# Kernel optimization log

Hardware: AMD Instinct MI355X
Metric: run time of the kernel (lower is better)

The kernel has to match this reference:

```python
import jax, jax.numpy as jnp
import numpy as np
from jax import lax

B, C, H, W = 128, 256, 32, 32
KH, KW = 8, 8


def depthwise_xcorr(x, kernel):
    """Depthwise cross-correlation: each (batch, channel) plane of x is
    correlated with the matching (batch, channel) plane of kernel,
    equivalent to F.conv2d(x.view(1,B*C,H,W), k.view(B*C,1,kh,kw), groups=B*C).
    Note torch conv2d is cross-correlation (no kernel flip), matching lax."""
    b, c, h, w = x.shape
    kh, kw = kernel.shape[2], kernel.shape[3]
    xr = x.reshape(1, b * c, h, w)
    kr = kernel.reshape(b * c, 1, kh, kw)
    out = lax.conv_general_dilated(
        xr, kr,
        window_strides=(1, 1),
        padding='VALID',
        dimension_numbers=('NCHW', 'OIHW', 'NCHW'),
        feature_group_count=b * c,
    )  # (1, b*c, h-kh+1, w-kw+1)
    return out.reshape(b, c, h - kh + 1, w - kw + 1)


def setup_inputs() -> dict:
    key = jax.random.key(0)
    k1, k2 = jax.random.split(key)
    x = jax.random.normal(k1, (B, C, H, W), dtype=jnp.float32)
    kernel = jax.random.normal(k2, (B, C, KH, KW), dtype=jnp.float32)
    weight = jnp.ones((3,), dtype=jnp.float32)  # nn.Parameter(torch.ones(channels))
    return {"x": x, "kernel": kernel, "weight": weight}


def reference(x, kernel, weight):
    # Original runs three identical depthwise-correlation implementations
    # (testCon2dSvf, testCon2dPSvf, F.conv2d) over the same data, then blends
    # with softmax weights. Since all three compute the same correlation,
    # out = (w0 + w1 + w2) * corr. We compute the correlation once.
    corr = depthwise_xcorr(x, kernel)
    w = jax.nn.softmax(weight, axis=0)
    return (w[0] + w[1] + w[2]) * corr
```

## Files before the change

kernel.cpp:

```cpp
#include <hip/hip_runtime.h>


#define NPLANES (128 * 256)
#define PPB 4
#define RST 18
#define XP  592
#define KTB (PPB * XP)
#define KTS 36
#define LDS_DW (KTB + PPB * KTS)
#define OH 25
#define OW 25

__device__ __forceinline__ unsigned cvt_pk_bf16(float a, float b) {
    unsigned r;
    asm("v_cvt_pk_bf16_f32 %0, %1, %2" : "=v"(r) : "v"(a), "v"(b));
    return r;
}
__device__ __forceinline__ void dot2(float& acc, unsigned x2, unsigned k2) {
    asm("v_dot2_f32_bf16 %0, %1, %2, %0" : "+v"(acc) : "v"(x2), "v"(k2));
}
__device__ __forceinline__ unsigned alignb(unsigned hi, unsigned lo, unsigned sh) {
    unsigned r;
    asm("v_alignbit_b32 %0, %1, %2, %3" : "=v"(r) : "v"(hi), "v"(lo), "v"(sh));
    return r;
}

__device__ __forceinline__ int plane_shift(int pl) {
    const int m = pl % 3;
    return (m == 0) ? 0 : (m == 1) ? 12 : 8;
}

__global__ __launch_bounds__(128)
void dwxcorr_kernel(const float* __restrict__ x,
                    const float* __restrict__ kern,
                    float* __restrict__ out) {
    __shared__ unsigned ldsu[LDS_DW];
    const int tid = threadIdx.x;
    const int plane0 = blockIdx.x * PPB;

#pragma unroll
    for (int it = 0; it < 2; ++it) {
        const int u    = tid + it * 128;
        const int pl   = u >> 6;
        const int rh   = u & 63;
        const int row  = rh >> 1;
        const int half = rh & 1;
        const float* g = x + (size_t)(plane0 + pl) * 1024 + row * 32 + half * 16;
        const float4 v0 = *reinterpret_cast<const float4*>(g + 0);
        const float4 v1 = *reinterpret_cast<const float4*>(g + 4);
        const float4 v2 = *reinterpret_cast<const float4*>(g + 8);
        const float4 v3 = *reinterpret_cast<const float4*>(g + 12);
        unsigned A[8];
        A[0] = cvt_pk_bf16(v0.x, v0.y); A[1] = cvt_pk_bf16(v0.z, v0.w);
        A[2] = cvt_pk_bf16(v1.x, v1.y); A[3] = cvt_pk_bf16(v1.z, v1.w);
        A[4] = cvt_pk_bf16(v2.x, v2.y); A[5] = cvt_pk_bf16(v2.z, v2.w);
        A[6] = cvt_pk_bf16(v3.x, v3.y); A[7] = cvt_pk_bf16(v3.z, v3.w);
        unsigned* base = &ldsu[pl * XP + plane_shift(pl) + row * RST + half * 8];
        *reinterpret_cast<uint2*>(base + 0) = make_uint2(A[0], A[1]);
        *reinterpret_cast<uint2*>(base + 2) = make_uint2(A[2], A[3]);
        *reinterpret_cast<uint2*>(base + 4) = make_uint2(A[4], A[5]);
        *reinterpret_cast<uint2*>(base + 6) = make_uint2(A[6], A[7]);
    }
    if (tid < PPB * 16) {
        const int pl = tid >> 4;
        const int o4 = tid & 15;
        const float4 v =
            *reinterpret_cast<const float4*>(kern + (size_t)(plane0 + pl) * 64 + o4 * 4);
        unsigned* kb = &ldsu[KTB + pl * KTS + o4 * 2];
        kb[0] = cvt_pk_bf16(v.x, v.y);
        kb[1] = cvt_pk_bf16(v.z, v.w);
    }
    __syncthreads();

    const int pb = tid / 25;
    if (pb >= PPB) return;
    const int ox = tid % 25;

    unsigned kt[32];
    {
        const unsigned* kp = &ldsu[KTB + pb * KTS];
#pragma unroll
        for (int i = 0; i < 8; ++i) {
            const uint4 q = *reinterpret_cast<const uint4*>(kp + 4 * i);
            kt[4*i+0] = q.x; kt[4*i+1] = q.y; kt[4*i+2] = q.z; kt[4*i+3] = q.w;
        }
    }

    float acc[OH];
#pragma unroll
    for (int i = 0; i < OH; ++i) acc[i] = 0.f;

    const unsigned sh = (ox & 1) * 16;
    const unsigned* xb = &ldsu[pb * XP + plane_shift(pb) + (ox >> 1)];
#pragma unroll
    for (int r = 0; r < 32; ++r) {
        const unsigned* rp = xb + r * RST;
        const unsigned d0 = rp[0], d1 = rp[1], d2 = rp[2], d3 = rp[3], d4 = rp[4];
        const unsigned w0 = alignb(d1, d0, sh);
        const unsigned w1 = alignb(d2, d1, sh);
        const unsigned w2 = alignb(d3, d2, sh);
        const unsigned w3 = alignb(d4, d3, sh);
#pragma unroll
        for (int ky = 0; ky < 8; ++ky) {
            const int oy = r - ky;
            if (oy >= 0 && oy < OH) {
                dot2(acc[oy], w0, kt[ky * 4 + 0]);
                dot2(acc[oy], w1, kt[ky * 4 + 1]);
                dot2(acc[oy], w2, kt[ky * 4 + 2]);
                dot2(acc[oy], w3, kt[ky * 4 + 3]);
            }
        }
    }

    float* op = out + (size_t)(plane0 + pb) * (OH * OW) + ox;
#pragma unroll
    for (int oy = 0; oy < OH; ++oy) op[oy * OW] = acc[oy];
}

extern "C" void kernel_launch(void* const* d_in, const int* in_sizes, int n_in,
                              void* d_out, int out_size, void* d_ws, size_t ws_size,
                              hipStream_t stream) {
    const float* x = (const float*)d_in[0];
    const float* k = (const float*)d_in[1];
    float* out = (float*)d_out;
    const int nblocks = NPLANES / PPB;
    dwxcorr_kernel<<<nblocks, 128, 0, stream>>>(x, k, out);
}
```

Baseline: 44.74 us.

## Double-buffer LDS and prefetch next plane group across persistent loop

Each block now handles four groups of four planes in a loop, issuing global loads for the next group into registers before computing the current group. It converts and writes them into a second LDS buffer afterwards, so memory latency overlaps with the dot2 compute. The grid shrinks by a factor of four and LDS per block doubles. Risks are higher register pressure from the held float4 prefetch values and less parallelism from fewer blocks.

Result: slower. 49.21 us (+10.0%).

```diff
diff --git a/kernel.cpp b/kernel.cpp
--- a/kernel.cpp
+++ b/kernel.cpp
@@ -3,11 +3,12 @@
 
 #define NPLANES (128 * 256)
 #define PPB 4
+#define NGRP 4
 #define RST 18
 #define XP  592
 #define KTB (PPB * XP)
 #define KTS 36
-#define LDS_DW (KTB + PPB * KTS)
+#define BUFDW (KTB + PPB * KTS)
 #define OH 25
 #define OW 25
 
@@ -24,7 +25,6 @@
     asm("v_alignbit_b32 %0, %1, %2, %3" : "=v"(r) : "v"(hi), "v"(lo), "v"(sh));
     return r;
 }
-
 __device__ __forceinline__ int plane_shift(int pl) {
     const int m = pl % 3;
     return (m == 0) ? 0 : (m == 1) ? 12 : 8;
@@ -34,87 +34,105 @@
 void dwxcorr_kernel(const float* __restrict__ x,
                     const float* __restrict__ kern,
                     float* __restrict__ out) {
-    __shared__ unsigned ldsu[LDS_DW];
+    __shared__ unsigned ldsu[2 * BUFDW];
     const int tid = threadIdx.x;
-    const int plane0 = blockIdx.x * PPB;
+    const int base_plane = blockIdx.x * (PPB * NGRP);
 
-#pragma unroll
-    for (int it = 0; it < 2; ++it) {
-        const int u    = tid + it * 128;
-        const int pl   = u >> 6;
-        const int rh   = u & 63;
-        const int row  = rh >> 1;
-        const int half = rh & 1;
-        const float* g = x + (size_t)(plane0 + pl) * 1024 + row * 32 + half * 16;
-        const float4 v0 = *reinterpret_cast<const float4*>(g + 0);
-        const float4 v1 = *reinterpret_cast<const float4*>(g + 4);
-        const float4 v2 = *reinterpret_cast<const float4*>(g + 8);
-        const float4 v3 = *reinterpret_cast<const float4*>(g + 12);
-        unsigned A[8];
-        A[0] = cvt_pk_bf16(v0.x, v0.y); A[1] = cvt_pk_bf16(v0.z, v0.w);
-        A[2] = cvt_pk_bf16(v1.x, v1.y); A[3] = cvt_pk_bf16(v1.z, v1.w);
-        A[4] = cvt_pk_bf16(v2.x, v2.y); A[5] = cvt_pk_bf16(v2.z, v2.w);
-        A[6] = cvt_pk_bf16(v3.x, v3.y); A[7] = cvt_pk_bf16(v3.z, v3.w);
-        unsigned* base = &ldsu[pl * XP + plane_shift(pl) + row * RST + half * 8];
-        *reinterpret_cast<uint2*>(base + 0) = make_uint2(A[0], A[1]);
-        *reinterpret_cast<uint2*>(base + 2) = make_uint2(A[2], A[3]);
-        *reinterpret_cast<uint2*>(base + 4) = make_uint2(A[4], A[5]);
-        *reinterpret_cast<uint2*>(base + 6) = make_uint2(A[6], A[7]);
-    }
-    if (tid < PPB * 16) {
-        const int pl = tid >> 4;
-        const int o4 = tid & 15;
-        const float4 v =
-            *reinterpret_cast<const float4*>(kern + (size_t)(plane0 + pl) * 64 + o4 * 4);
-        unsigned* kb = &ldsu[KTB + pl * KTS + o4 * 2];
-        kb[0] = cvt_pk_bf16(v.x, v.y);
-        kb[1] = cvt_pk_bf16(v.z, v.w);
-    }
+    const int pl0 = tid >> 6,  rh0 = tid & 63,  row0 = rh0 >> 1, half0 = rh0 & 1;
+    const int u1  = tid + 128;
+    const int pl1 = u1 >> 6,   rh1 = u1 & 63,   row1 = rh1 >> 1, half1 = rh1 & 1;
+    const int tpl = tid >> 4,  to4 = tid & 15;
+
+    float4 a0, a1, a2, a3, b0, b1, b2, b3, tp;
+
+#define LOADX(g) do {                                                          \
+        const size_t p_ = (size_t)(base_plane + (g) * PPB);                    \
+        const float* g0_ = x + (p_ + pl0) * 1024 + row0 * 32 + half0 * 16;     \
+        a0 = *(const float4*)(g0_ + 0);  a1 = *(const float4*)(g0_ + 4);       \
+        a2 = *(const float4*)(g0_ + 8);  a3 = *(const float4*)(g0_ + 12);      \
+        const float* g1_ = x + (p_ + pl1) * 1024 + row1 * 32 + half1 * 16;     \
+        b0 = *(const float4*)(g1_ + 0);  b1 = *(const float4*)(g1_ + 4);       \
+        b2 = *(const float4*)(g1_ + 8);  b3 = *(const float4*)(g1_ + 12);      \
+        if (tid < PPB * 16)                                                    \
+            tp = *((const float4*)kern + (p_ + tpl) * 16 + to4);               \
+    } while (0)
+
+#define WRITEX(buf) do {                                                       \
+        unsigned* L_ = &ldsu[(buf) * BUFDW];                                   \
+        unsigned* w0_ = &L_[pl0 * XP + plane_shift(pl0) + row0 * RST + half0 * 8]; \
+        *(uint2*)(w0_ + 0) = make_uint2(cvt_pk_bf16(a0.x, a0.y), cvt_pk_bf16(a0.z, a0.w)); \
+        *(uint2*)(w0_ + 2) = make_uint2(cvt_pk_bf16(a1.x, a1.y), cvt_pk_bf16(a1.z, a1.w)); \
+        *(uint2*)(w0_ + 4) = make_uint2(cvt_pk_bf16(a2.x, a2.y), cvt_pk_bf16(a2.z, a2.w)); \
+        *(uint2*)(w0_ + 6) = make_uint2(cvt_pk_bf16(a3.x, a3.y), cvt_pk_bf16(a3.z, a3.w)); \
+        unsigned* w1_ = &L_[pl1 * XP + plane_shift(pl1) + row1 * RST + half1 * 8]; \
+        *(uint2*)(w1_ + 0) = make_uint2(cvt_pk_bf16(b0.x, b0.y), cvt_pk_bf16(b0.z, b0.w)); \
+        *(uint2*)(w1_ + 2) = make_uint2(cvt_pk_bf16(b1.x, b1.y), cvt_pk_bf16(b1.z, b1.w)); \
+        *(uint2*)(w1_ + 4) = make_uint2(cvt_pk_bf16(b2.x, b2.y), cvt_pk_bf16(b2.z, b2.w)); \
+        *(uint2*)(w1_ + 6) = make_uint2(cvt_pk_bf16(b3.x, b3.y), cvt_pk_bf16(b3.z, b3.w)); \
+        if (tid < PPB * 16) {                                                  \
+            unsigned* kb_ = &L_[KTB + tpl * KTS + to4 * 2];                    \
+            kb_[0] = cvt_pk_bf16(tp.x, tp.y);                                  \
+            kb_[1] = cvt_pk_bf16(tp.z, tp.w);                                  \
+        }                                                                      \
+    } while (0)
+
+    LOADX(0);
+    WRITEX(0);
     __syncthreads();
 
     const int pb = tid / 25;
-    if (pb >= PPB) return;
     const int ox = tid % 25;
+    const unsigned sh = (ox & 1) * 16;
 
-    unsigned kt[32];
-    {
-        const unsigned* kp = &ldsu[KTB + pb * KTS];
+#pragma unroll 1
+    for (int g = 0; g < NGRP; ++g) {
+        if (g + 1 < NGRP) LOADX(g + 1);
+
+        if (pb < PPB) {
+            const unsigned* L = &ldsu[(g & 1) * BUFDW];
+            unsigned kt[32];
+            {
+                const unsigned* kp = &L[KTB + pb * KTS];
 #pragma unroll
-        for (int i = 0; i < 8; ++i) {
-            const uint4 q = *reinterpret_cast<const uint4*>(kp + 4 * i);
-            kt[4*i+0] = q.x; kt[4*i+1] = q.y; kt[4*i+2] = q.z; kt[4*i+3] = q.w;
+                for (int i = 0; i < 8; ++i) {
+                    const uint4 q = *reinterpret_cast<const uint4*>(kp + 4 * i);
+                    kt[4*i+0] = q.x; kt[4*i+1] = q.y; kt[4*i+2] = q.z; kt[4*i+3] = q.w;
+                }
+            }
+            float acc[OH];
+#pragma unroll
+            for (int i = 0; i < OH; ++i) acc[i] = 0.f;
+
+            const unsigned* xb = &L[pb * XP + plane_shift(pb) + (ox >> 1)];
+#pragma unroll
+            for (int r = 0; r < 32; ++r) {
+                const unsigned* rp = xb + r * RST;
+                const unsigned d0 = rp[0], d1 = rp[1], d2 = rp[2], d3 = rp[3], d4 = rp[4];
+                const unsigned w0 = alignb(d1, d0, sh);
+                const unsigned w1 = alignb(d2, d1, sh);
+                const unsigned w2 = alignb(d3, d2, sh);
+                const unsigned w3 = alignb(d4, d3, sh);
+#pragma unroll
+                for (int ky = 0; ky < 8; ++ky) {
+                    const int oy = r - ky;
+                    if (oy >= 0 && oy < OH) {
+                        dot2(acc[oy], w0, kt[ky * 4 + 0]);
+                        dot2(acc[oy], w1, kt[ky * 4 + 1]);
+                        dot2(acc[oy], w2, kt[ky * 4 + 2]);
+                        dot2(acc[oy], w3, kt[ky * 4 + 3]);
+                    }
+                }
+            }
+            float* op = out + (size_t)(base_plane + g * PPB + pb) * (OH * OW) + ox;
+#pragma unroll
+            for (int oy = 0; oy < OH; ++oy) op[oy * OW] = acc[oy];
         }
+
+        if (g + 1 < NGRP) WRITEX((g + 1) & 1);
+        __syncthreads();
     }
-
-    float acc[OH];
-#pragma unroll
-    for (int i = 0; i < OH; ++i) acc[i] = 0.f;
-
-    const unsigned sh = (ox & 1) * 16;
-    const unsigned* xb = &ldsu[pb * XP + plane_shift(pb) + (ox >> 1)];
-#pragma unroll
-    for (int r = 0; r < 32; ++r) {
-        const unsigned* rp = xb + r * RST;
-        const unsigned d0 = rp[0], d1 = rp[1], d2 = rp[2], d3 = rp[3], d4 = rp[4];
-        const unsigned w0 = alignb(d1, d0, sh);
-        const unsigned w1 = alignb(d2, d1, sh);
-        const unsigned w2 = alignb(d3, d2, sh);
-        const unsigned w3 = alignb(d4, d3, sh);
-#pragma unroll
-        for (int ky = 0; ky < 8; ++ky) {
-            const int oy = r - ky;
-            if (oy >= 0 && oy < OH) {
-                dot2(acc[oy], w0, kt[ky * 4 + 0]);
-                dot2(acc[oy], w1, kt[ky * 4 + 1]);
-                dot2(acc[oy], w2, kt[ky * 4 + 2]);
-                dot2(acc[oy], w3, kt[ky * 4 + 3]);
-            }
-        }
-    }
-
-    float* op = out + (size_t)(plane0 + pb) * (OH * OW) + ox;
-#pragma unroll
-    for (int oy = 0; oy < OH; ++oy) op[oy * OW] = acc[oy];
+#undef LOADX
+#undef WRITEX
 }
 
 extern "C" void kernel_launch(void* const* d_in, const int* in_sizes, int n_in,
@@ -123,6 +141,6 @@
     const float* x = (const float*)d_in[0];
     const float* k = (const float*)d_in[1];
     float* out = (float*)d_out;
-    const int nblocks = NPLANES / PPB;
+    const int nblocks = NPLANES / (PPB * NGRP);
     dwxcorr_kernel<<<nblocks, 128, 0, stream>>>(x, k, out);
 }
```
